# Optimization experiments

Hardware: AMD Instinct MI355X
Metric: run time of the kernel (lower is better)

Reference implementation:

```python
import jax, jax.numpy as jnp
import numpy as np

IN_DIM = 128
SLOT_SIZE = 64
NUM_SLOTS = 8
NUM_ITERS = 3
MLP_HDIM = 128
EPSILON = 1e-08


def _layernorm(x, g, b, eps=1e-5):
    m = jnp.mean(x, axis=-1, keepdims=True)
    v = jnp.mean((x - m) ** 2, axis=-1, keepdims=True)
    return (x - m) * jax.lax.rsqrt(v + eps) * g + b


def setup_inputs() -> dict:
    key = jax.random.key(0)
    ks = jax.random.split(key, 16)
    H, D, K, M = SLOT_SIZE, IN_DIM, NUM_SLOTS, MLP_HDIM
    x = jax.random.normal(ks[0], (32, 4096, D), dtype=jnp.float32)
    noise = jax.random.normal(ks[1], (32, K, H), dtype=jnp.float32)
    s = lambda k, shape, fan_in: jax.random.normal(k, shape, jnp.float32) * (1.0 / np.sqrt(fan_in))
    return {
        'x': x,
        'noise': noise,
        'Wq': s(ks[2], (H, H), H),            # project_q (no bias)
        'Wk': s(ks[3], (H, D), D),            # project_k
        'Wv': s(ks[4], (H, D), D),            # project_v
        'ln_in_g': jnp.ones((D,), jnp.float32), 'ln_in_b': jnp.zeros((D,), jnp.float32),
        'ln_sl_g': jnp.ones((H,), jnp.float32), 'ln_sl_b': jnp.zeros((H,), jnp.float32),
        'ln_mlp_g': jnp.ones((H,), jnp.float32), 'ln_mlp_b': jnp.zeros((H,), jnp.float32),
        'gru_w_ih': s(ks[5], (3 * H, H), H),  # PyTorch GRUCell weight_ih (r,z,n)
        'gru_w_hh': s(ks[6], (3 * H, H), H),
        'gru_b_ih': jnp.zeros((3 * H,), jnp.float32),
        'gru_b_hh': jnp.zeros((3 * H,), jnp.float32),
        'mlp_w1': s(ks[7], (M, H), H), 'mlp_b1': jnp.zeros((M,), jnp.float32),
        'mlp_w2': s(ks[8], (H, M), M), 'mlp_b2': jnp.zeros((H,), jnp.float32),
        'slots_mu': jnp.tile(jnp.linspace(-1.0, 1.0, K, dtype=jnp.float32)[None, :, None], (1, 1, H)),
        'slots_logsigma': jnp.full((1, K, H), -1.0, dtype=jnp.float32),
    }


def reference(x, noise, Wq, Wk, Wv, ln_in_g, ln_in_b, ln_sl_g, ln_sl_b,
              ln_mlp_g, ln_mlp_b, gru_w_ih, gru_w_hh, gru_b_ih, gru_b_hh,
              mlp_w1, mlp_b1, mlp_w2, mlp_b2, slots_mu, slots_logsigma):
    B = x.shape[0]
    H, K = SLOT_SIZE, NUM_SLOTS
    xn = _layernorm(x, ln_in_g, ln_in_b)
    k = jnp.einsum('bnd,hd->bnh', xn, Wk)  # [B,N,H]
    v = jnp.einsum('bnd,hd->bnh', xn, Wv)

    scale = jax.nn.softplus(slots_logsigma) + 1e-05
    slots = slots_mu + scale * noise  # rsample, broadcast over batch -> [B,K,H]

    def step(slots):
        slots_prev = slots
        s = _layernorm(slots, ln_sl_g, ln_sl_b)
        q = jnp.einsum('bkh,gh->bkg', s, Wq)  # [B,K,H]
        scores = (H ** -0.5) * jnp.einsum('bnh,bkh->bnk', k, q)
        attn = jax.nn.softmax(scores, axis=-1) + EPSILON  # softmax over slots
        attn = attn / jnp.sum(attn, axis=1, keepdims=True)  # normalize over inputs
        updates = jnp.einsum('bnk,bnh->bkh', attn, v)
        # PyTorch GRUCell: gates ordered (r, z, n)
        u = updates.reshape(-1, H)
        h = slots_prev.reshape(-1, H)
        gx = u @ gru_w_ih.T + gru_b_ih
        gh = h @ gru_w_hh.T + gru_b_hh
        xr, xz, xn_ = jnp.split(gx, 3, axis=-1)
        hr, hz, hn = jnp.split(gh, 3, axis=-1)
        r = jax.nn.sigmoid(xr + hr)
        z = jax.nn.sigmoid(xz + hz)
        n = jnp.tanh(xn_ + r * hn)
        slots = ((1.0 - z) * n + z * h).reshape(B, K, H)
        slots = _layernorm(slots, ln_mlp_g, ln_mlp_b)
        mlp_out = jax.nn.relu(slots @ mlp_w1.T + mlp_b1) @ mlp_w2.T + mlp_b2
        return slots + mlp_out

    for _ in range(NUM_ITERS):
        slots = step(slots)
    return slots
```

## Files before the change

kernel.cpp:

```cpp
#include <hip/hip_runtime.h>

typedef __attribute__((ext_vector_type(8))) short s16x8;
typedef __attribute__((ext_vector_type(4))) float f32x4;

#define DEV static __device__ __forceinline__

DEV float b2f(unsigned short u){
  unsigned int i = ((unsigned int)u) << 16;
  float f; __builtin_memcpy(&f, &i, 4); return f;
}
DEV unsigned short f2b(float f){
  unsigned int i; __builtin_memcpy(&i, &f, 4);
  i = i + 0x7fffu + ((i >> 16) & 1u);
  return (unsigned short)(i >> 16);
}
DEV f32x4 mfma16(s16x8 a, s16x8 b, f32x4 c){
  return __builtin_amdgcn_mfma_f32_16x16x32_bf16(a, b, c, 0, 0, 0);
}
DEV s16x8 ld8f(const float* p){
  const float4* q4 = (const float4*)p;
  float4 a = q4[0], b = q4[1];
  s16x8 r;
  r[0]=(short)f2b(a.x); r[1]=(short)f2b(a.y); r[2]=(short)f2b(a.z); r[3]=(short)f2b(a.w);
  r[4]=(short)f2b(b.x); r[5]=(short)f2b(b.y); r[6]=(short)f2b(b.z); r[7]=(short)f2b(b.w);
  return r;
}

template<int C> DEV float dpp_addstep(float x){
  int y = __builtin_amdgcn_update_dpp(0, __builtin_bit_cast(int, x), C, 0xF, 0xF, true);
  return x + __builtin_bit_cast(float, y);
}
DEV float rsum16(float v){
  v = dpp_addstep<0xB1>(v);
  v = dpp_addstep<0x4E>(v);
  v = dpp_addstep<0x141>(v);
  v = dpp_addstep<0x140>(v);
  return v;
}

__global__ __launch_bounds__(256) void k_wpack(
    const float* __restrict__ Wk, const float* __restrict__ Wv,
    const float* __restrict__ wih, const float* __restrict__ whh,
    const float* __restrict__ w1, const float* __restrict__ w2,
    const float* __restrict__ Wq,
    unsigned short* __restrict__ wkb, unsigned short* __restrict__ wvb,
    unsigned short* __restrict__ wall)
{
  int t = blockIdx.x * 256 + threadIdx.x;
  int off = t * 4;
  const float* src; unsigned short* dst;
  if      (off <  8192){ src = Wk  + off;         dst = wkb  + off; }
  else if (off < 16384){ src = Wv  + off -  8192; dst = wvb  + off - 8192; }
  else if (off < 28672){ src = wih + off - 16384; dst = wall + off - 16384; }
  else if (off < 40960){ src = whh + off - 28672; dst = wall + off - 16384; }
  else if (off < 49152){ src = w1  + off - 40960; dst = wall + off - 16384; }
  else if (off < 57344){ src = w2  + off - 49152; dst = wall + off - 16384; }
  else                 { src = Wq  + off - 57344; dst = wall + off - 16384; }
  float4 v = *(const float4*)src;
  ushort4 o;
  o.x = f2b(v.x); o.y = f2b(v.y); o.z = f2b(v.z); o.w = f2b(v.w);
  *(ushort4*)dst = o;
}

__global__ __launch_bounds__(256, 4) void k_lnkv5(
    const float* __restrict__ x,
    const unsigned short* __restrict__ wkb,
    const unsigned short* __restrict__ wvb,
    const float* __restrict__ lg,
    const float* __restrict__ lb,
    unsigned short* __restrict__ kg,
    unsigned short* __restrict__ vt,
    const float* __restrict__ noise,
    const float* __restrict__ mu,
    const float* __restrict__ lsg,
    const float* __restrict__ gsl,
    const float* __restrict__ bsl,
    const float* __restrict__ Wq,
    float* __restrict__ slots,
    unsigned short* __restrict__ qws)
{
  __shared__ __align__(16) unsigned int xs[128 * 68];
  const int tid = threadIdx.x;
  const int w = tid >> 6, ln = tid & 63;
  const int m16 = ln & 15, q = ln >> 4;

  if (blockIdx.x >= 1024){
    unsigned short* st = (unsigned short*)xs;
    float (*redS)[4] = (float(*)[4])((char*)xs + 2304);
    float (*redQ)[4] = (float(*)[4])((char*)xs + 2560);
    const int bi = blockIdx.x - 1024;
    const int r0 = bi * 16;
    const int cw = w*16 + m16;

    float sl[4], s1[4], s2[4];
    #pragma unroll
    for (int rr = 0; rr < 4; ++rr){
      int row = r0 + q*4 + rr;
      int k = row & 7;
      float v = mu[k*64 + cw] + (log1pf(expf(lsg[k*64 + cw])) + 1e-5f) * noise[row*64 + cw];
      sl[rr] = v;
      slots[row*64 + cw] = v;
      s1[rr] = rsum16(v);
      s2[rr] = rsum16(v*v);
    }
    if (m16 == 0){
      #pragma unroll
      for (int rr = 0; rr < 4; ++rr){ redS[q*4+rr][w] = s1[rr]; redQ[q*4+rr][w] = s2[rr]; }
    }
    __syncthreads();
    {
      const float gs = gsl[cw], bs = bsl[cw];
      #pragma unroll
      for (int rr = 0; rr < 4; ++rr){
        f32x4 aS = *(const f32x4*)redS[q*4+rr];
        f32x4 aQ = *(const f32x4*)redQ[q*4+rr];
        float tS = aS[0]+aS[1]+aS[2]+aS[3];
        float tQ = aQ[0]+aQ[1]+aQ[2]+aQ[3];
        float mean = tS*(1.f/64.f);
        float var  = tQ*(1.f/64.f) - mean*mean;
        float rs = rsqrtf(var + 1e-5f);
        float sq = (sl[rr] - mean)*rs*gs + bs;
        st[(q*4+rr)*72 + cw] = f2b(sq);
      }
    }
    __syncthreads();
    {
      f32x4 acc = {0,0,0,0};
      #pragma unroll
      for (int ks = 0; ks < 2; ++ks){
        s16x8 a = *(const s16x8*)(st + m16*72 + ks*32 + q*8);
        acc = mfma16(a, ld8f(Wq + cw*64 + ks*32 + q*8), acc);
      }
      #pragma unroll
      for (int rr = 0; rr < 4; ++rr){
        int row = r0 + q*4 + rr;
        int bb_ = row >> 3, kk = row & 7;
        qws[(bb_*16 + kk)*64 + cw] = f2b(acc[rr] * 0.125f);
      }
      int b0 = bi * 2;
      ((unsigned int*)(qws + (b0*16 + 8)*64))[tid] = 0u;
      ((unsigned int*)(qws + ((b0+1)*16 + 8)*64))[tid] = 0u;
    }
    return;
  }

  const int b = blockIdx.x >> 5;
  const int nbase = (blockIdx.x & 31) << 7;
  const long rowg0 = (long)b * 4096 + nbase;

  {
    const int c = m16;
    const float4 gA = *(const float4*)(lg + c*4);
    const float4 gB = *(const float4*)(lg + 64 + c*4);
    const float4 bA = *(const float4*)(lb + c*4);
    const float4 bB = *(const float4*)(lb + 64 + c*4);
    const float* base = x + (rowg0 + w*32 + q)*128;

    float4 va[2], vb[2];
    va[0] = *(const float4*)(base + c*4);
    vb[0] = *(const float4*)(base + 64 + c*4);
    #pragma unroll
    for (int p = 0; p < 8; ++p){
      const int cur = p & 1, nxt = cur ^ 1;
      if (p < 7){
        va[nxt] = *(const float4*)(base + (p+1)*512 + c*4);
        vb[nxt] = *(const float4*)(base + (p+1)*512 + 64 + c*4);
      }
      float4 u = va[cur], t = vb[cur];
      float s1 = (u.x + u.y) + (u.z + u.w) + (t.x + t.y) + (t.z + t.w);
      float s2 = (u.x*u.x + u.y*u.y) + (u.z*u.z + u.w*u.w)
               + (t.x*t.x + t.y*t.y) + (t.z*t.z + t.w*t.w);
      s1 = rsum16(s1);
      s2 = rsum16(s2);
      float mean = s1 * (1.f/128.f);
      float var  = s2 * (1.f/128.f) - mean*mean;
      float rs = rsqrtf(var + 1e-5f);
      float y0 = (u.x - mean)*rs*gA.x + bA.x;
      float y1 = (u.y - mean)*rs*gA.y + bA.y;
      float y2 = (u.z - mean)*rs*gA.z + bA.z;
      float y3 = (u.w - mean)*rs*gA.w + bA.w;
      float y4 = (t.x - mean)*rs*gB.x + bB.x;
      float y5 = (t.y - mean)*rs*gB.y + bB.y;
      float y6 = (t.z - mean)*rs*gB.z + bB.z;
      float y7 = (t.w - mean)*rs*gB.w + bB.w;
      uint2 pkA, pkB;
      pkA.x = (unsigned int)f2b(y0) | ((unsigned int)f2b(y1) << 16);
      pkA.y = (unsigned int)f2b(y2) | ((unsigned int)f2b(y3) << 16);
      pkB.x = (unsigned int)f2b(y4) | ((unsigned int)f2b(y5) << 16);
      pkB.y = (unsigned int)f2b(y6) | ((unsigned int)f2b(y7) << 16);
      const int r = w*32 + p*4 + q;
      *(uint2*)&xs[r*68 + c*2] = pkA;
      *(uint2*)&xs[r*68 + 32 + c*2] = pkB;
    }
  }

  s16x8 bw[4][4];
  #pragma unroll
  for (int t = 0; t < 4; ++t)
    #pragma unroll
    for (int kb = 0; kb < 4; ++kb)
      bw[kb][t] = *(const s16x8*)(wkb + (t*16 + m16)*128 + kb*32 + q*8);

  __syncthreads();

  const f32x4 zf = {0.f, 0.f, 0.f, 0.f};

  #pragma unroll
  for (int mi = 0; mi < 2; ++mi){
    int n0 = (w*2 + mi) * 16;
    f32x4 acc[4];
    #pragma unroll
    for (int t = 0; t < 4; ++t) acc[t] = zf;
    #pragma unroll
    for (int kb = 0; kb < 4; ++kb){
      s16x8 af = *(const s16x8*)((const unsigned short*)(xs + (n0 + m16)*68) + kb*32 + q*8);
      #pragma unroll
      for (int t = 0; t < 4; ++t)
        acc[t] = mfma16(af, bw[kb][t], acc[t]);
    }
    #pragma unroll
    for (int t = 0; t < 4; ++t){
      int h = t*16 + m16;
      #pragma unroll
      for (int rr = 0; rr < 4; ++rr){
        long n = rowg0 + n0 + q*4 + rr;
        kg[n*64 + h] = f2b(acc[t][rr]);
      }
    }
  }

  #pragma unroll
  for (int t = 0; t < 4; ++t)
    #pragma unroll
    for (int kb = 0; kb < 4; ++kb)
      bw[kb][t] = *(const s16x8*)(wvb + (t*16 + m16)*128 + kb*32 + q*8);

  #pragma unroll
  for (int mi = 0; mi < 2; ++mi){
    int n0 = (w*2 + mi) * 16;
    f32x4 acc[4];
    #pragma unroll
    for (int t = 0; t < 4; ++t) acc[t] = zf;
    #pragma unroll
    for (int kb = 0; kb < 4; ++kb){
      s16x8 af = *(const s16x8*)((const unsigned short*)(xs + (n0 + m16)*68) + kb*32 + q*8);
      #pragma unroll
      for (int t = 0; t < 4; ++t)
        acc[t] = mfma16(af, bw[kb][t], acc[t]);
    }
    #pragma unroll
    for (int t = 0; t < 4; ++t){
      int h = t*16 + m16;
      unsigned int p0 = (unsigned int)f2b(acc[t][0]) | ((unsigned int)f2b(acc[t][1]) << 16);
      unsigned int p1 = (unsigned int)f2b(acc[t][2]) | ((unsigned int)f2b(acc[t][3]) << 16);
      uint2 pv; pv.x = p0; pv.y = p1;
      long off = ((long)b*64 + h)*4096 + nbase + n0 + q*4;
      *(uint2*)(vt + off) = pv;
    }
  }
}

__global__ __launch_bounds__(256) void k_attn3(
    const unsigned short* __restrict__ kg,
    const unsigned short* __restrict__ vt,
    const unsigned short* __restrict__ qws,
    const unsigned short* __restrict__ wall,
    const float* __restrict__ bih, const float* __restrict__ bhh,
    const float* __restrict__ b1p, const float* __restrict__ b2p,
    const float* __restrict__ gmlp, const float* __restrict__ bmlp,
    const float* __restrict__ gsl, const float* __restrict__ bsl,
    const float* __restrict__ Up_in, const float* __restrict__ Sp_in,
    float* __restrict__ Up_out, float* __restrict__ Sp_out,
    const float* __restrict__ slin, float* __restrict__ slout,
    int it)
{
  __shared__ float sc[256*17];
  __shared__ unsigned short aT[16*264];
  __shared__ unsigned short ut[16*72], ht[16*72], st[16*72], hid[16*136];
  __shared__ unsigned short qloc[16*72];
  __shared__ __align__(16) float redS[16][4];
  __shared__ __align__(16) float redQ[16][4];
  __shared__ __align__(16) float redS2[16][4];
  __shared__ __align__(16) float redQ2[16][4];

  const int tid = threadIdx.x;
  const int w = tid >> 6, ln = tid & 63;
  const int m16 = ln & 15, q = ln >> 4;
  const int b = blockIdx.x >> 4;
  const int tile = blockIdx.x & 15;
  const int nbase = tile << 8;

  s16x8 afp[4];
  #pragma unroll
  for (int mi = 0; mi < 4; ++mi){
    int n0 = (w*4 + mi)*16;
    afp[mi] = *(const s16x8*)(kg + ((long)b*4096 + nbase + n0 + m16)*64 + q*8);
  }
  s16x8 afp2[4];
  #pragma unroll
  for (int mi = 0; mi < 4; ++mi){
    int n0 = (w*4 + mi)*16;
    afp2[mi] = *(const s16x8*)(kg + ((long)b*4096 + nbase + n0 + m16)*64 + 32 + q*8);
  }
  s16x8 vtp[8];
  #pragma unroll
  for (int ks = 0; ks < 8; ++ks)
    vtp[ks] = *(const s16x8*)(vt + ((long)b*64 + w*16 + m16)*4096 + nbase + ks*32 + q*8);

  for (int i = tid; i < 8*264; i += 256) aT[8*264 + i] = 0;
  if (tid < 128){
    int row = 8 + (tid >> 4), c = (tid & 15)*4;
    ushort4 z4 = {0,0,0,0};
    *(ushort4*)&qloc[row*72 + c] = z4;
  }

  if (it == 0){
    if (tid < 128){
      int row = tid >> 4, c = (tid & 15)*4;
      *(ushort4*)&qloc[row*72 + c] = *(const ushort4*)(qws + (b*16 + row)*64 + c);
    }
  } else {
    const int r0 = (b >> 1) * 16;
    const int cw = w*16 + m16;
    const unsigned short* wihb = wall;
    const unsigned short* whhb = wall + 12288;
    const unsigned short* w1b  = wall + 24576;
    const unsigned short* w2b  = wall + 32768;
    const unsigned short* wqb  = wall + 40960;

    #pragma unroll
    for (int p = 0; p < 4; ++p){
      int row = p*4 + w;
      int g = r0 + row;
      int bb = g >> 3, sl = g & 7;
      const float* up  = Up_in + ((bb*16)*8 + sl)*64 + ln;
      const float* spp = Sp_in + (bb*16)*8 + sl;
      float usum = 0.f, ssum = 0.f;
      #pragma unroll
      for (int t = 0; t < 16; ++t){
        usum += up[t*512];
        ssum += spp[t*8];
      }
      ut[row*72 + ln] = f2b(usum / ssum);
      ht[row*72 + ln] = f2b(slin[g*64 + ln]);
    }
    __syncthreads();

    f32x4 axr = {0,0,0,0}, axz = {0,0,0,0}, axn = {0,0,0,0};
    f32x4 ahr = {0,0,0,0}, ahz = {0,0,0,0}, ahn = {0,0,0,0};
    #pragma unroll
    for (int ks = 0; ks < 2; ++ks){
      s16x8 au = *(const s16x8*)(ut + m16*72 + ks*32 + q*8);
      s16x8 ah = *(const s16x8*)(ht + m16*72 + ks*32 + q*8);
      axr = mfma16(au, *(const s16x8*)(wihb + (      cw)*64 + ks*32 + q*8), axr);
      axz = mfma16(au, *(const s16x8*)(wihb + ( 64 + cw)*64 + ks*32 + q*8), axz);
      axn = mfma16(au, *(const s16x8*)(wihb + (128 + cw)*64 + ks*32 + q*8), axn);
      ahr = mfma16(ah, *(const s16x8*)(whhb + (      cw)*64 + ks*32 + q*8), ahr);
      ahz = mfma16(ah, *(const s16x8*)(whhb + ( 64 + cw)*64 + ks*32 + q*8), ahz);
      ahn = mfma16(ah, *(const s16x8*)(whhb + (128 + cw)*64 + ks*32 + q*8), ahn);
    }
    const float bxr = bih[cw], bxz = bih[64+cw], bxn = bih[128+cw];
    const float bhr = bhh[cw], bhz = bhh[64+cw], bhn = bhh[128+cw];
    float sp[4];
    #pragma unroll
    for (int rr = 0; rr < 4; ++rr){
      float xr = axr[rr] + bxr, xz = axz[rr] + bxz, xnv = axn[rr] + bxn;
      float hr = ahr[rr] + bhr, hz = ahz[rr] + bhz, hn = ahn[rr] + bhn;
      float rg = 1.f / (1.f + expf(-(xr + hr)));
      float zg = 1.f / (1.f + expf(-(xz + hz)));
      float ng = tanhf(xnv + rg*hn);
      float hv = b2f(ht[(q*4 + rr)*72 + cw]);
      sp[rr] = (1.f - zg)*ng + zg*hv;
    }

    float s1[4], s2[4];
    #pragma unroll
    for (int rr = 0; rr < 4; ++rr){
      s1[rr] = rsum16(sp[rr]);
      s2[rr] = rsum16(sp[rr]*sp[rr]);
    }
    if (m16 == 0){
      #pragma unroll
      for (int rr = 0; rr < 4; ++rr){ redS[q*4+rr][w] = s1[rr]; redQ[q*4+rr][w] = s2[rr]; }
    }
    __syncthreads();
    float sl_[4];
    {
      const float gm = gmlp[cw], bm = bmlp[cw];
      #pragma unroll
      for (int rr = 0; rr < 4; ++rr){
        f32x4 aS = *(const f32x4*)redS[q*4+rr];
        f32x4 aQ = *(const f32x4*)redQ[q*4+rr];
        float tS = aS[0]+aS[1]+aS[2]+aS[3];
        float tQ = aQ[0]+aQ[1]+aQ[2]+aQ[3];
        float mean = tS*(1.f/64.f);
        float var  = tQ*(1.f/64.f) - mean*mean;
        float rs = rsqrtf(var + 1e-5f);
        sl_[rr] = (sp[rr] - mean)*rs*gm + bm;
        st[(q*4+rr)*72 + cw] = f2b(sl_[rr]);
      }
    }
    __syncthreads();

    #pragma unroll
    for (int t2 = 0; t2 < 2; ++t2){
      int nt = w*2 + t2;
      int col = nt*16 + m16;
      f32x4 acc = {0,0,0,0};
      #pragma unroll
      for (int ks = 0; ks < 2; ++ks){
        s16x8 a = *(const s16x8*)(st + m16*72 + ks*32 + q*8);
        acc = mfma16(a, *(const s16x8*)(w1b + col*64 + ks*32 + q*8), acc);
      }
      float bb = b1p[col];
      #pragma unroll
      for (int rr = 0; rr < 4; ++rr)
        hid[(q*4+rr)*136 + col] = f2b(fmaxf(acc[rr] + bb, 0.f));
    }
    __syncthreads();

    float snew[4];
    {
      f32x4 acc = {0,0,0,0};
      #pragma unroll
      for (int ks = 0; ks < 4; ++ks){
        s16x8 a = *(const s16x8*)(hid + m16*136 + ks*32 + q*8);
        acc = mfma16(a, *(const s16x8*)(w2b + cw*128 + ks*32 + q*8), acc);
      }
      float bb = b2p[cw];
      #pragma unroll
      for (int rr = 0; rr < 4; ++rr){
        snew[rr] = sl_[rr] + acc[rr] + bb;
        if ((blockIdx.x & 31) == 0)
          slout[(r0 + q*4 + rr)*64 + cw] = snew[rr];
      }
    }

    #pragma unroll
    for (int rr = 0; rr < 4; ++rr){
      s1[rr] = rsum16(snew[rr]);
      s2[rr] = rsum16(snew[rr]*snew[rr]);
    }
    if (m16 == 0){
      #pragma unroll
      for (int rr = 0; rr < 4; ++rr){ redS2[q*4+rr][w] = s1[rr]; redQ2[q*4+rr][w] = s2[rr]; }
    }
    __syncthreads();
    {
      const float gs = gsl[cw], bs = bsl[cw];
      #pragma unroll
      for (int rr = 0; rr < 4; ++rr){
        f32x4 aS = *(const f32x4*)redS2[q*4+rr];
        f32x4 aQ = *(const f32x4*)redQ2[q*4+rr];
        float tS = aS[0]+aS[1]+aS[2]+aS[3];
        float tQ = aQ[0]+aQ[1]+aQ[2]+aQ[3];
        float mean = tS*(1.f/64.f);
        float var  = tQ*(1.f/64.f) - mean*mean;
        float rs = rsqrtf(var + 1e-5f);
        float sq = (snew[rr] - mean)*rs*gs + bs;
        st[(q*4+rr)*72 + cw] = f2b(sq);
      }
    }
    __syncthreads();
    {
      f32x4 acc = {0,0,0,0};
      #pragma unroll
      for (int ks = 0; ks < 2; ++ks){
        s16x8 a = *(const s16x8*)(st + m16*72 + ks*32 + q*8);
        acc = mfma16(a, *(const s16x8*)(wqb + cw*64 + ks*32 + q*8), acc);
      }
      #pragma unroll
      for (int rr = 0; rr < 4; ++rr){
        int rloc = q*4 + rr;
        if ((rloc >> 3) == (b & 1))
          qloc[(rloc & 7)*72 + cw] = f2b(acc[rr] * 0.125f);
      }
    }
  }
  __syncthreads();

  s16x8 bq[2];
  #pragma unroll
  for (int ks = 0; ks < 2; ++ks)
    bq[ks] = *(const s16x8*)(qloc + m16*72 + ks*32 + q*8);

  #pragma unroll
  for (int mi = 0; mi < 4; ++mi){
    int n0 = (w*4 + mi)*16;
    f32x4 acc = {0.f, 0.f, 0.f, 0.f};
    acc = mfma16(afp[mi],  bq[0], acc);
    acc = mfma16(afp2[mi], bq[1], acc);
    #pragma unroll
    for (int rr = 0; rr < 4; ++rr)
      sc[(n0 + q*4 + rr)*17 + m16] = acc[rr];
  }
  __syncthreads();

  {
    int r = tid;
    float a8[8];
    float mx = -1e30f;
    #pragma unroll
    for (int j = 0; j < 8; ++j){ a8[j] = sc[r*17 + j]; mx = fmaxf(mx, a8[j]); }
    float ssum = 0.f;
    #pragma unroll
    for (int j = 0; j < 8; ++j){ a8[j] = expf(a8[j] - mx); ssum += a8[j]; }
    float inv = 1.f/ssum;
    #pragma unroll
    for (int j = 0; j < 8; ++j)
      aT[j*264 + r] = f2b(a8[j]*inv + 1e-8f);
  }
  __syncthreads();

  {
    int j = tid >> 5, c = tid & 31;
    float p = 0.f;
    #pragma unroll
    for (int i = 0; i < 8; ++i) p += b2f(aT[j*264 + c + 32*i]);
    p = rsum16(p);
    p += __shfl_xor(p, 16);
    if ((tid & 31) == 0) Sp_out[(b*16 + tile)*8 + j] = p;
  }

  {
    f32x4 acc = {0.f, 0.f, 0.f, 0.f};
    #pragma unroll
    for (int ks = 0; ks < 8; ++ks){
      s16x8 af = *(const s16x8*)(aT + m16*264 + ks*32 + q*8);
      acc = mfma16(af, vtp[ks], acc);
    }
    float* ub = Up_out + ((b*16 + tile)*8)*64 + w*16 + m16;
    #pragma unroll
    for (int rr = 0; rr < 4; ++rr){
      int slot = q*4 + rr;
      if (slot < 8)
        ub[slot*64] = acc[rr];
    }
  }
}

__global__ __launch_bounds__(256) void k_gru2(
    const float* __restrict__ Up, const float* __restrict__ Sp,
    const float* __restrict__ slots,
    const float* __restrict__ wih, const float* __restrict__ whh,
    const float* __restrict__ bih, const float* __restrict__ bhh,
    const float* __restrict__ w1, const float* __restrict__ b1p,
    const float* __restrict__ w2, const float* __restrict__ b2p,
    const float* __restrict__ gmlp, const float* __restrict__ bmlp,
    float* __restrict__ outp)
{
  __shared__ unsigned short ut[16*72], ht[16*72], st[16*72], hid[16*136];
  __shared__ __align__(16) float redS[16][4];
  __shared__ __align__(16) float redQ[16][4];
  const int tid = threadIdx.x;
  const int w = tid >> 6, ln = tid & 63;
  const int m16 = ln & 15, q = ln >> 4;
  const int r0 = blockIdx.x * 16;
  const int cw = w*16 + m16;

  #pragma unroll
  for (int p = 0; p < 4; ++p){
    int row = p*4 + w;
    int g = r0 + row;
    int bb = g >> 3, sl = g & 7;
    const float* up  = Up + ((bb*16)*8 + sl)*64 + ln;
    const float* spp = Sp + (bb*16)*8 + sl;
    float usum = 0.f, ssum = 0.f;
    #pragma unroll
    for (int t = 0; t < 16; ++t){
      usum += up[t*512];
      ssum += spp[t*8];
    }
    ut[row*72 + ln] = f2b(usum / ssum);
    ht[row*72 + ln] = f2b(slots[g*64 + ln]);
  }
  __syncthreads();

  f32x4 axr = {0,0,0,0}, axz = {0,0,0,0}, axn = {0,0,0,0};
  f32x4 ahr = {0,0,0,0}, ahz = {0,0,0,0}, ahn = {0,0,0,0};
  #pragma unroll
  for (int ks = 0; ks < 2; ++ks){
    s16x8 au = *(const s16x8*)(ut + m16*72 + ks*32 + q*8);
    s16x8 ah = *(const s16x8*)(ht + m16*72 + ks*32 + q*8);
    axr = mfma16(au, ld8f(wih + (      cw)*64 + ks*32 + q*8), axr);
    axz = mfma16(au, ld8f(wih + ( 64 + cw)*64 + ks*32 + q*8), axz);
    axn = mfma16(au, ld8f(wih + (128 + cw)*64 + ks*32 + q*8), axn);
    ahr = mfma16(ah, ld8f(whh + (      cw)*64 + ks*32 + q*8), ahr);
    ahz = mfma16(ah, ld8f(whh + ( 64 + cw)*64 + ks*32 + q*8), ahz);
    ahn = mfma16(ah, ld8f(whh + (128 + cw)*64 + ks*32 + q*8), ahn);
  }
  const float bxr = bih[cw], bxz = bih[64+cw], bxn = bih[128+cw];
  const float bhr = bhh[cw], bhz = bhh[64+cw], bhn = bhh[128+cw];
  float sp[4];
  #pragma unroll
  for (int rr = 0; rr < 4; ++rr){
    float xr = axr[rr] + bxr, xz = axz[rr] + bxz, xnv = axn[rr] + bxn;
    float hr = ahr[rr] + bhr, hz = ahz[rr] + bhz, hn = ahn[rr] + bhn;
    float rg = 1.f / (1.f + expf(-(xr + hr)));
    float zg = 1.f / (1.f + expf(-(xz + hz)));
    float ng = tanhf(xnv + rg*hn);
    float hv = b2f(ht[(q*4 + rr)*72 + cw]);
    sp[rr] = (1.f - zg)*ng + zg*hv;
  }

  float s1[4], s2[4];
  #pragma unroll
  for (int rr = 0; rr < 4; ++rr){
    s1[rr] = rsum16(sp[rr]);
    s2[rr] = rsum16(sp[rr]*sp[rr]);
  }
  if (m16 == 0){
    #pragma unroll
    for (int rr = 0; rr < 4; ++rr){ redS[q*4+rr][w] = s1[rr]; redQ[q*4+rr][w] = s2[rr]; }
  }
  __syncthreads();
  float sl_[4];
  {
    const float gm = gmlp[cw], bm = bmlp[cw];
    #pragma unroll
    for (int rr = 0; rr < 4; ++rr){
      f32x4 aS = *(const f32x4*)redS[q*4+rr];
      f32x4 aQ = *(const f32x4*)redQ[q*4+rr];
      float tS = aS[0]+aS[1]+aS[2]+aS[3];
      float tQ = aQ[0]+aQ[1]+aQ[2]+aQ[3];
      float mean = tS*(1.f/64.f);
      float var  = tQ*(1.f/64.f) - mean*mean;
      float rs = rsqrtf(var + 1e-5f);
      sl_[rr] = (sp[rr] - mean)*rs*gm + bm;
      st[(q*4+rr)*72 + cw] = f2b(sl_[rr]);
    }
  }
  __syncthreads();

  #pragma unroll
  for (int t2 = 0; t2 < 2; ++t2){
    int nt = w*2 + t2;
    int col = nt*16 + m16;
    f32x4 acc = {0,0,0,0};
    #pragma unroll
    for (int ks = 0; ks < 2; ++ks){
      s16x8 a = *(const s16x8*)(st + m16*72 + ks*32 + q*8);
      acc = mfma16(a, ld8f(w1 + col*64 + ks*32 + q*8), acc);
    }
    float bb = b1p[col];
    #pragma unroll
    for (int rr = 0; rr < 4; ++rr)
      hid[(q*4+rr)*136 + col] = f2b(fmaxf(acc[rr] + bb, 0.f));
  }
  __syncthreads();

  {
    f32x4 acc = {0,0,0,0};
    #pragma unroll
    for (int ks = 0; ks < 4; ++ks){
      s16x8 a = *(const s16x8*)(hid + m16*136 + ks*32 + q*8);
      acc = mfma16(a, ld8f(w2 + cw*128 + ks*32 + q*8), acc);
    }
    float bb = b2p[cw];
    #pragma unroll
    for (int rr = 0; rr < 4; ++rr){
      int row = r0 + q*4 + rr;
      outp[row*64 + cw] = sl_[rr] + acc[rr] + bb;
    }
  }
}

extern "C" void kernel_launch(void* const* d_in, const int* in_sizes, int n_in,
                              void* d_out, int out_size, void* d_ws, size_t ws_size,
                              hipStream_t stream)
{
  const float* x    = (const float*)d_in[0];
  const float* noise= (const float*)d_in[1];
  const float* Wq   = (const float*)d_in[2];
  const float* Wk   = (const float*)d_in[3];
  const float* Wv   = (const float*)d_in[4];
  const float* ling = (const float*)d_in[5];
  const float* linb = (const float*)d_in[6];
  const float* gsl  = (const float*)d_in[7];
  const float* bsl  = (const float*)d_in[8];
  const float* gmlp = (const float*)d_in[9];
  const float* bmlp = (const float*)d_in[10];
  const float* wih  = (const float*)d_in[11];
  const float* whh  = (const float*)d_in[12];
  const float* bih  = (const float*)d_in[13];
  const float* bhh  = (const float*)d_in[14];
  const float* w1   = (const float*)d_in[15];
  const float* b1p  = (const float*)d_in[16];
  const float* w2   = (const float*)d_in[17];
  const float* b2p  = (const float*)d_in[18];
  const float* mu   = (const float*)d_in[19];
  const float* lsg  = (const float*)d_in[20];

  char* ws = (char*)d_ws;
  unsigned short* kg   = (unsigned short*)(ws);
  unsigned short* vt   = (unsigned short*)(ws + 16777216);
  char* base = ws + 33554432;
  unsigned short* qws  = (unsigned short*)(base);
  float* slotsA        = (float*)(base + 65536);
  float* slotsB        = (float*)(base + 131072);
  float* slotsC        = (float*)(base + 196608);
  float* UA            = (float*)(base + 262144);
  float* UB            = (float*)(base + 1310720);
  float* SA            = (float*)(base + 2359296);
  float* SB            = (float*)(base + 2375680);
  unsigned short* wkb  = (unsigned short*)(base + 2392064);
  unsigned short* wvb  = (unsigned short*)(base + 2408448);
  unsigned short* wall = (unsigned short*)(base + 2424832);
  float* outp          = (float*)d_out;

  hipLaunchKernelGGL(k_wpack, dim3(60), dim3(256), 0, stream,
                     Wk, Wv, wih, whh, w1, w2, Wq, wkb, wvb, wall);
  hipLaunchKernelGGL(k_lnkv5, dim3(1040), dim3(256), 0, stream,
                     x, wkb, wvb, ling, linb, kg, vt,
                     noise, mu, lsg, gsl, bsl, Wq, slotsA, qws);
  hipLaunchKernelGGL(k_attn3, dim3(512), dim3(256), 0, stream,
                     kg, vt, qws, wall, bih, bhh, b1p, b2p, gmlp, bmlp, gsl, bsl,
                     UA, SA, UA, SA, slotsA, slotsA, 0);
  hipLaunchKernelGGL(k_attn3, dim3(512), dim3(256), 0, stream,
                     kg, vt, qws, wall, bih, bhh, b1p, b2p, gmlp, bmlp, gsl, bsl,
                     UA, SA, UB, SB, slotsA, slotsB, 1);
  hipLaunchKernelGGL(k_attn3, dim3(512), dim3(256), 0, stream,
                     kg, vt, qws, wall, bih, bhh, b1p, b2p, gmlp, bmlp, gsl, bsl,
                     UB, SB, UA, SA, slotsB, slotsC, 2);
  hipLaunchKernelGGL(k_gru2, dim3(16), dim3(256), 0, stream, UA, SA, slotsC,
                     wih, whh, bih, bhh, w1, b1p, w2, b2p, gmlp, bmlp, outp);
  (void)in_sizes; (void)n_in; (void)out_size; (void)ws_size;
}
```

Measured before the change: 201.9 us.

## Fuse three attention iterations and final GRU into one persistent kernel with grid barrier

Replaces the three k_attn3 launches and the k_gru2 launch with a single persistent k_iter kernel that loops over the iterations and separates them with a software grid-wide atomic barrier. The final GRU/MLP runs in the first 16 blocks after the last barrier. K and V fragments are no longer held in registers across phases; they are reloaded from global memory inside each iteration. Triple-buffered U/S partials avoid read/write races across iterations. The aim is to cut kernel-launch gaps and tail effects, at the risk of spin-wait cost, possible deadlock if not all 512 blocks are co-resident, and repeated global loads.

```diff
diff --git a/kernel.cpp b/kernel.cpp
--- a/kernel.cpp
+++ b/kernel.cpp
@@ -38,14 +38,36 @@
   return v;
 }
 
+DEV void gridbar(unsigned int* bar, unsigned int nblk){
+  __syncthreads();
+  if (threadIdx.x == 0){
+    __threadfence();
+    unsigned int g = __hip_atomic_load(&bar[1], __ATOMIC_RELAXED, __HIP_MEMORY_SCOPE_AGENT);
+    unsigned int old = __hip_atomic_fetch_add(&bar[0], 1u, __ATOMIC_ACQ_REL, __HIP_MEMORY_SCOPE_AGENT);
+    if (old == nblk - 1u){
+      __hip_atomic_store(&bar[0], 0u, __ATOMIC_RELAXED, __HIP_MEMORY_SCOPE_AGENT);
+      __hip_atomic_store(&bar[1], g + 1u, __ATOMIC_RELEASE, __HIP_MEMORY_SCOPE_AGENT);
+    } else {
+      int tries = 0;
+      while (__hip_atomic_load(&bar[1], __ATOMIC_ACQUIRE, __HIP_MEMORY_SCOPE_AGENT) == g){
+        if (++tries > (1 << 24)) break;
+      }
+    }
+    __threadfence();
+  }
+  __syncthreads();
+}
+
 __global__ __launch_bounds__(256) void k_wpack(
     const float* __restrict__ Wk, const float* __restrict__ Wv,
     const float* __restrict__ wih, const float* __restrict__ whh,
     const float* __restrict__ w1, const float* __restrict__ w2,
     const float* __restrict__ Wq,
     unsigned short* __restrict__ wkb, unsigned short* __restrict__ wvb,
-    unsigned short* __restrict__ wall)
+    unsigned short* __restrict__ wall,
+    unsigned int* __restrict__ bar)
 {
+  if (blockIdx.x == 0 && threadIdx.x == 0){ bar[0] = 0u; bar[1] = 0u; }
   int t = blockIdx.x * 256 + threadIdx.x;
   int off = t * 4;
   const float* src; unsigned short* dst;
@@ -260,7 +282,7 @@
   }
 }
 
-__global__ __launch_bounds__(256) void k_attn3(
+__global__ __launch_bounds__(256, 4) void k_iter(
     const unsigned short* __restrict__ kg,
     const unsigned short* __restrict__ vt,
     const unsigned short* __restrict__ qws,
@@ -269,10 +291,12 @@
     const float* __restrict__ b1p, const float* __restrict__ b2p,
     const float* __restrict__ gmlp, const float* __restrict__ bmlp,
     const float* __restrict__ gsl, const float* __restrict__ bsl,
-    const float* __restrict__ Up_in, const float* __restrict__ Sp_in,
-    float* __restrict__ Up_out, float* __restrict__ Sp_out,
-    const float* __restrict__ slin, float* __restrict__ slout,
-    int it)
+    float* __restrict__ U0, float* __restrict__ U1, float* __restrict__ U2,
+    float* __restrict__ S0, float* __restrict__ S1, float* __restrict__ S2,
+    float* __restrict__ slotsA, float* __restrict__ slotsB,
+    float* __restrict__ slotsC,
+    float* __restrict__ outp,
+    unsigned int* __restrict__ bar)
 {
   __shared__ float sc[256*17];
   __shared__ unsigned short aT[16*264];
@@ -289,23 +313,13 @@
   const int b = blockIdx.x >> 4;
   const int tile = blockIdx.x & 15;
   const int nbase = tile << 8;
-
-  s16x8 afp[4];
-  #pragma unroll
-  for (int mi = 0; mi < 4; ++mi){
-    int n0 = (w*4 + mi)*16;
-    afp[mi] = *(const s16x8*)(kg + ((long)b*4096 + nbase + n0 + m16)*64 + q*8);
-  }
-  s16x8 afp2[4];
-  #pragma unroll
-  for (int mi = 0; mi < 4; ++mi){
-    int n0 = (w*4 + mi)*16;
-    afp2[mi] = *(const s16x8*)(kg + ((long)b*4096 + nbase + n0 + m16)*64 + 32 + q*8);
-  }
-  s16x8 vtp[8];
-  #pragma unroll
-  for (int ks = 0; ks < 8; ++ks)
-    vtp[ks] = *(const s16x8*)(vt + ((long)b*64 + w*16 + m16)*4096 + nbase + ks*32 + q*8);
+  const int cw = w*16 + m16;
+
+  const unsigned short* wihb = wall;
+  const unsigned short* whhb = wall + 12288;
+  const unsigned short* w1b  = wall + 24576;
+  const unsigned short* w2b  = wall + 32768;
+  const unsigned short* wqb  = wall + 40960;
 
   for (int i = tid; i < 8*264; i += 256) aT[8*264 + i] = 0;
   if (tid < 128){
@@ -314,27 +328,250 @@
     *(ushort4*)&qloc[row*72 + c] = z4;
   }
 
-  if (it == 0){
-    if (tid < 128){
-      int row = tid >> 4, c = (tid & 15)*4;
-      *(ushort4*)&qloc[row*72 + c] = *(const ushort4*)(qws + (b*16 + row)*64 + c);
-    }
-  } else {
-    const int r0 = (b >> 1) * 16;
-    const int cw = w*16 + m16;
-    const unsigned short* wihb = wall;
-    const unsigned short* whhb = wall + 12288;
-    const unsigned short* w1b  = wall + 24576;
-    const unsigned short* w2b  = wall + 32768;
-    const unsigned short* wqb  = wall + 40960;
+  for (int it = 0; it < 3; ++it){
+    const float* Up_in  = (it == 1) ? U0 : U1;
+    const float* Sp_in  = (it == 1) ? S0 : S1;
+    float*       Up_out = (it == 0) ? U0 : ((it == 1) ? U1 : U2);
+    float*       Sp_out = (it == 0) ? S0 : ((it == 1) ? S1 : S2);
+    const float* slin   = (it == 1) ? slotsA : slotsB;
+    float*       slout  = (it == 1) ? slotsB : slotsC;
+
+    if (it == 0){
+      if (tid < 128){
+        int row = tid >> 4, c = (tid & 15)*4;
+        *(ushort4*)&qloc[row*72 + c] = *(const ushort4*)(qws + (b*16 + row)*64 + c);
+      }
+    } else {
+      const int r0 = (b >> 1) * 16;
+
+      #pragma unroll
+      for (int p = 0; p < 4; ++p){
+        int row = p*4 + w;
+        int g = r0 + row;
+        int bb = g >> 3, sl = g & 7;
+        const float* up  = Up_in + ((bb*16)*8 + sl)*64 + ln;
+        const float* spp = Sp_in + (bb*16)*8 + sl;
+        float usum = 0.f, ssum = 0.f;
+        #pragma unroll
+        for (int t = 0; t < 16; ++t){
+          usum += up[t*512];
+          ssum += spp[t*8];
+        }
+        ut[row*72 + ln] = f2b(usum / ssum);
+        ht[row*72 + ln] = f2b(slin[g*64 + ln]);
+      }
+      __syncthreads();
+
+      f32x4 axr = {0,0,0,0}, axz = {0,0,0,0}, axn = {0,0,0,0};
+      f32x4 ahr = {0,0,0,0}, ahz = {0,0,0,0}, ahn = {0,0,0,0};
+      #pragma unroll
+      for (int ks = 0; ks < 2; ++ks){
+        s16x8 au = *(const s16x8*)(ut + m16*72 + ks*32 + q*8);
+        s16x8 ah = *(const s16x8*)(ht + m16*72 + ks*32 + q*8);
+        axr = mfma16(au, *(const s16x8*)(wihb + (      cw)*64 + ks*32 + q*8), axr);
+        axz = mfma16(au, *(const s16x8*)(wihb + ( 64 + cw)*64 + ks*32 + q*8), axz);
+        axn = mfma16(au, *(const s16x8*)(wihb + (128 + cw)*64 + ks*32 + q*8), axn);
+        ahr = mfma16(ah, *(const s16x8*)(whhb + (      cw)*64 + ks*32 + q*8), ahr);
+        ahz = mfma16(ah, *(const s16x8*)(whhb + ( 64 + cw)*64 + ks*32 + q*8), ahz);
+        ahn = mfma16(ah, *(const s16x8*)(whhb + (128 + cw)*64 + ks*32 + q*8), ahn);
+      }
+      const float bxr = bih[cw], bxz = bih[64+cw], bxn = bih[128+cw];
+      const float bhr = bhh[cw], bhz = bhh[64+cw], bhn = bhh[128+cw];
+      float sp[4];
+      #pragma unroll
+      for (int rr = 0; rr < 4; ++rr){
+        float xr = axr[rr] + bxr, xz = axz[rr] + bxz, xnv = axn[rr] + bxn;
+        float hr = ahr[rr] + bhr, hz = ahz[rr] + bhz, hn = ahn[rr] + bhn;
+        float rg = 1.f / (1.f + expf(-(xr + hr)));
+        float zg = 1.f / (1.f + expf(-(xz + hz)));
+        float ng = tanhf(xnv + rg*hn);
+        float hv = b2f(ht[(q*4 + rr)*72 + cw]);
+        sp[rr] = (1.f - zg)*ng + zg*hv;
+      }
+
+      float s1[4], s2[4];
+      #pragma unroll
+      for (int rr = 0; rr < 4; ++rr){
+        s1[rr] = rsum16(sp[rr]);
+        s2[rr] = rsum16(sp[rr]*sp[rr]);
+      }
+      if (m16 == 0){
+        #pragma unroll
+        for (int rr = 0; rr < 4; ++rr){ redS[q*4+rr][w] = s1[rr]; redQ[q*4+rr][w] = s2[rr]; }
+      }
+      __syncthreads();
+      float sl_[4];
+      {
+        const float gm = gmlp[cw], bm = bmlp[cw];
+        #pragma unroll
+        for (int rr = 0; rr < 4; ++rr){
+          f32x4 aS = *(const f32x4*)redS[q*4+rr];
+          f32x4 aQ = *(const f32x4*)redQ[q*4+rr];
+          float tS = aS[0]+aS[1]+aS[2]+aS[3];
+          float tQ = aQ[0]+aQ[1]+aQ[2]+aQ[3];
+          float mean = tS*(1.f/64.f);
+          float var  = tQ*(1.f/64.f) - mean*mean;
+          float rs = rsqrtf(var + 1e-5f);
+          sl_[rr] = (sp[rr] - mean)*rs*gm + bm;
+          st[(q*4+rr)*72 + cw] = f2b(sl_[rr]);
+        }
+      }
+      __syncthreads();
+
+      #pragma unroll
+      for (int t2 = 0; t2 < 2; ++t2){
+        int nt = w*2 + t2;
+        int col = nt*16 + m16;
+        f32x4 acc = {0,0,0,0};
+        #pragma unroll
+        for (int ks = 0; ks < 2; ++ks){
+          s16x8 a = *(const s16x8*)(st + m16*72 + ks*32 + q*8);
+          acc = mfma16(a, *(const s16x8*)(w1b + col*64 + ks*32 + q*8), acc);
+        }
+        float bb = b1p[col];
+        #pragma unroll
+        for (int rr = 0; rr < 4; ++rr)
+          hid[(q*4+rr)*136 + col] = f2b(fmaxf(acc[rr] + bb, 0.f));
+      }
+      __syncthreads();
+
+      float snew[4];
+      {
+        f32x4 acc = {0,0,0,0};
+        #pragma unroll
+        for (int ks = 0; ks < 4; ++ks){
+          s16x8 a = *(const s16x8*)(hid + m16*136 + ks*32 + q*8);
+          acc = mfma16(a, *(const s16x8*)(w2b + cw*128 + ks*32 + q*8), acc);
+        }
+        float bb = b2p[cw];
+        #pragma unroll
+        for (int rr = 0; rr < 4; ++rr){
+          snew[rr] = sl_[rr] + acc[rr] + bb;
+          if ((blockIdx.x & 31) == 0)
+            slout[(r0 + q*4 + rr)*64 + cw] = snew[rr];
+        }
+      }
+
+      #pragma unroll
+      for (int rr = 0; rr < 4; ++rr){
+        s1[rr] = rsum16(snew[rr]);
+        s2[rr] = rsum16(snew[rr]*snew[rr]);
+      }
+      if (m16 == 0){
+        #pragma unroll
+        for (int rr = 0; rr < 4; ++rr){ redS2[q*4+rr][w] = s1[rr]; redQ2[q*4+rr][w] = s2[rr]; }
+      }
+      __syncthreads();
+      {
+        const float gs = gsl[cw], bs = bsl[cw];
+        #pragma unroll
+        for (int rr = 0; rr < 4; ++rr){
+          f32x4 aS = *(const f32x4*)redS2[q*4+rr];
+          f32x4 aQ = *(const f32x4*)redQ2[q*4+rr];
+          float tS = aS[0]+aS[1]+aS[2]+aS[3];
+          float tQ = aQ[0]+aQ[1]+aQ[2]+aQ[3];
+          float mean = tS*(1.f/64.f);
+          float var  = tQ*(1.f/64.f) - mean*mean;
+          float rs = rsqrtf(var + 1e-5f);
+          float sq = (snew[rr] - mean)*rs*gs + bs;
+          st[(q*4+rr)*72 + cw] = f2b(sq);
+        }
+      }
+      __syncthreads();
+      {
+        f32x4 acc = {0,0,0,0};
+        #pragma unroll
+        for (int ks = 0; ks < 2; ++ks){
+          s16x8 a = *(const s16x8*)(st + m16*72 + ks*32 + q*8);
+          acc = mfma16(a, *(const s16x8*)(wqb + cw*64 + ks*32 + q*8), acc);
+        }
+        #pragma unroll
+        for (int rr = 0; rr < 4; ++rr){
+          int rloc = q*4 + rr;
+          if ((rloc >> 3) == (b & 1))
+            qloc[(rloc & 7)*72 + cw] = f2b(acc[rr] * 0.125f);
+        }
+      }
+    }
+    __syncthreads();
+
+    s16x8 bq[2];
+    #pragma unroll
+    for (int ks = 0; ks < 2; ++ks)
+      bq[ks] = *(const s16x8*)(qloc + m16*72 + ks*32 + q*8);
+
+    #pragma unroll
+    for (int mi = 0; mi < 4; ++mi){
+      int n0 = (w*4 + mi)*16;
+      f32x4 acc = {0.f, 0.f, 0.f, 0.f};
+      #pragma unroll
+      for (int ks = 0; ks < 2; ++ks){
+        s16x8 af = *(const s16x8*)(kg + ((long)b*4096 + nbase + n0 + m16)*64 + ks*32 + q*8);
+        acc = mfma16(af, bq[ks], acc);
+      }
+      #pragma unroll
+      for (int rr = 0; rr < 4; ++rr)
+        sc[(n0 + q*4 + rr)*17 + m16] = acc[rr];
+    }
+    __syncthreads();
+
+    {
+      int r = tid;
+      float a8[8];
+      float mx = -1e30f;
+      #pragma unroll
+      for (int j = 0; j < 8; ++j){ a8[j] = sc[r*17 + j]; mx = fmaxf(mx, a8[j]); }
+      float ssum = 0.f;
+      #pragma unroll
+      for (int j = 0; j < 8; ++j){ a8[j] = expf(a8[j] - mx); ssum += a8[j]; }
+      float inv = 1.f/ssum;
+      #pragma unroll
+      for (int j = 0; j < 8; ++j)
+        aT[j*264 + r] = f2b(a8[j]*inv + 1e-8f);
+    }
+    __syncthreads();
+
+    {
+      int j = tid >> 5, c = tid & 31;
+      float p = 0.f;
+      #pragma unroll
+      for (int i = 0; i < 8; ++i) p += b2f(aT[j*264 + c + 32*i]);
+      p = rsum16(p);
+      p += __shfl_xor(p, 16);
+      if ((tid & 31) == 0) Sp_out[(b*16 + tile)*8 + j] = p;
+    }
+
+    {
+      f32x4 acc = {0.f, 0.f, 0.f, 0.f};
+      #pragma unroll
+      for (int ks = 0; ks < 8; ++ks){
+        s16x8 af = *(const s16x8*)(aT + m16*264 + ks*32 + q*8);
+        s16x8 bf = *(const s16x8*)(vt + ((long)b*64 + w*16 + m16)*4096 + nbase + ks*32 + q*8);
+        acc = mfma16(af, bf, acc);
+      }
+      float* ub = Up_out + ((b*16 + tile)*8)*64 + w*16 + m16;
+      #pragma unroll
+      for (int rr = 0; rr < 4; ++rr){
+        int slot = q*4 + rr;
+        if (slot < 8)
+          ub[slot*64] = acc[rr];
+      }
+    }
+
+    gridbar(bar, 512u);
+  }
+
+  if (blockIdx.x >= 16) return;
+  {
+    const int r0 = blockIdx.x * 16;
 
     #pragma unroll
     for (int p = 0; p < 4; ++p){
       int row = p*4 + w;
       int g = r0 + row;
       int bb = g >> 3, sl = g & 7;
-      const float* up  = Up_in + ((bb*16)*8 + sl)*64 + ln;
-      const float* spp = Sp_in + (bb*16)*8 + sl;
+      const float* up  = U2 + ((bb*16)*8 + sl)*64 + ln;
+      const float* spp = S2 + (bb*16)*8 + sl;
       float usum = 0.f, ssum = 0.f;
       #pragma unroll
       for (int t = 0; t < 16; ++t){
@@ -342,7 +579,7 @@
         ssum += spp[t*8];
       }
       ut[row*72 + ln] = f2b(usum / ssum);
-      ht[row*72 + ln] = f2b(slin[g*64 + ln]);
+      ht[row*72 + ln] = f2b(slotsC[g*64 + ln]);
     }
     __syncthreads();
 
@@ -419,7 +656,6 @@
     }
     __syncthreads();
 
-    float snew[4];
     {
       f32x4 acc = {0,0,0,0};
       #pragma unroll
@@ -430,237 +666,9 @@
       float bb = b2p[cw];
       #pragma unroll
       for (int rr = 0; rr < 4; ++rr){
-        snew[rr] = sl_[rr] + acc[rr] + bb;
-        if ((blockIdx.x & 31) == 0)
-          slout[(r0 + q*4 + rr)*64 + cw] = snew[rr];
-      }
-    }
-
-    #pragma unroll
-    for (int rr = 0; rr < 4; ++rr){
-      s1[rr] = rsum16(snew[rr]);
-      s2[rr] = rsum16(snew[rr]*snew[rr]);
-    }
-    if (m16 == 0){
-      #pragma unroll
-      for (int rr = 0; rr < 4; ++rr){ redS2[q*4+rr][w] = s1[rr]; redQ2[q*4+rr][w] = s2[rr]; }
-    }
-    __syncthreads();
-    {
-      const float gs = gsl[cw], bs = bsl[cw];
-      #pragma unroll
-      for (int rr = 0; rr < 4; ++rr){
-        f32x4 aS = *(const f32x4*)redS2[q*4+rr];
-        f32x4 aQ = *(const f32x4*)redQ2[q*4+rr];
-        float tS = aS[0]+aS[1]+aS[2]+aS[3];
-        float tQ = aQ[0]+aQ[1]+aQ[2]+aQ[3];
-        float mean = tS*(1.f/64.f);
-        float var  = tQ*(1.f/64.f) - mean*mean;
-        float rs = rsqrtf(var + 1e-5f);
-        float sq = (snew[rr] - mean)*rs*gs + bs;
-        st[(q*4+rr)*72 + cw] = f2b(sq);
-      }
-    }
-    __syncthreads();
-    {
-      f32x4 acc = {0,0,0,0};
-      #pragma unroll
-      for (int ks = 0; ks < 2; ++ks){
-        s16x8 a = *(const s16x8*)(st + m16*72 + ks*32 + q*8);
-        acc = mfma16(a, *(const s16x8*)(wqb + cw*64 + ks*32 + q*8), acc);
-      }
-      #pragma unroll
-      for (int rr = 0; rr < 4; ++rr){
-        int rloc = q*4 + rr;
-        if ((rloc >> 3) == (b & 1))
-          qloc[(rloc & 7)*72 + cw] = f2b(acc[rr] * 0.125f);
-      }
-    }
-  }
-  __syncthreads();
-
-  s16x8 bq[2];
-  #pragma unroll
-  for (int ks = 0; ks < 2; ++ks)
-    bq[ks] = *(const s16x8*)(qloc + m16*72 + ks*32 + q*8);
-
-  #pragma unroll
-  for (int mi = 0; mi < 4; ++mi){
-    int n0 = (w*4 + mi)*16;
-    f32x4 acc = {0.f, 0.f, 0.f, 0.f};
-    acc = mfma16(afp[mi],  bq[0], acc);
-    acc = mfma16(afp2[mi], bq[1], acc);
-    #pragma unroll
-    for (int rr = 0; rr < 4; ++rr)
-      sc[(n0 + q*4 + rr)*17 + m16] = acc[rr];
-  }
-  __syncthreads();
-
-  {
-    int r = tid;
-    float a8[8];
-    float mx = -1e30f;
-    #pragma unroll
-    for (int j = 0; j < 8; ++j){ a8[j] = sc[r*17 + j]; mx = fmaxf(mx, a8[j]); }
-    float ssum = 0.f;
-    #pragma unroll
-    for (int j = 0; j < 8; ++j){ a8[j] = expf(a8[j] - mx); ssum += a8[j]; }
-    float inv = 1.f/ssum;
-    #pragma unroll
-    for (int j = 0; j < 8; ++j)
-      aT[j*264 + r] = f2b(a8[j]*inv + 1e-8f);
-  }
-  __syncthreads();
-
-  {
-    int j = tid >> 5, c = tid & 31;
-    float p = 0.f;
-    #pragma unroll
-    for (int i = 0; i < 8; ++i) p += b2f(aT[j*264 + c + 32*i]);
-    p = rsum16(p);
-    p += __shfl_xor(p, 16);
-    if ((tid & 31) == 0) Sp_out[(b*16 + tile)*8 + j] = p;
-  }
-
-  {
-    f32x4 acc = {0.f, 0.f, 0.f, 0.f};
-    #pragma unroll
-    for (int ks = 0; ks < 8; ++ks){
-      s16x8 af = *(const s16x8*)(aT + m16*264 + ks*32 + q*8);
-      acc = mfma16(af, vtp[ks], acc);
-    }
-    float* ub = Up_out + ((b*16 + tile)*8)*64 + w*16 + m16;
-    #pragma unroll
-    for (int rr = 0; rr < 4; ++rr){
-      int slot = q*4 + rr;
-      if (slot < 8)
-        ub[slot*64] = acc[rr];
-    }
-  }
-}
-
-__global__ __launch_bounds__(256) void k_gru2(
-    const float* __restrict__ Up, const float* __restrict__ Sp,
-    const float* __restrict__ slots,
-    const float* __restrict__ wih, const float* __restrict__ whh,
-    const float* __restrict__ bih, const float* __restrict__ bhh,
-    const float* __restrict__ w1, const float* __restrict__ b1p,
-    const float* __restrict__ w2, const float* __restrict__ b2p,
-    const float* __restrict__ gmlp, const float* __restrict__ bmlp,
-    float* __restrict__ outp)
-{
-  __shared__ unsigned short ut[16*72], ht[16*72], st[16*72], hid[16*136];
-  __shared__ __align__(16) float redS[16][4];
-  __shared__ __align__(16) float redQ[16][4];
-  const int tid = threadIdx.x;
-  const int w = tid >> 6, ln = tid & 63;
-  const int m16 = ln & 15, q = ln >> 4;
-  const int r0 = blockIdx.x * 16;
-  const int cw = w*16 + m16;
-
-  #pragma unroll
-  for (int p = 0; p < 4; ++p){
-    int row = p*4 + w;
-    int g = r0 + row;
-    int bb = g >> 3, sl = g & 7;
-    const float* up  = Up + ((bb*16)*8 + sl)*64 + ln;
-    const float* spp = Sp + (bb*16)*8 + sl;
-    float usum = 0.f, ssum = 0.f;
-    #pragma unroll
-    for (int t = 0; t < 16; ++t){
-      usum += up[t*512];
-      ssum += spp[t*8];
-    }
-    ut[row*72 + ln] = f2b(usum / ssum);
-    ht[row*72 + ln] = f2b(slots[g*64 + ln]);
-  }
-  __syncthreads();
-
-  f32x4 axr = {0,0,0,0}, axz = {0,0,0,0}, axn = {0,0,0,0};
-  f32x4 ahr = {0,0,0,0}, ahz = {0,0,0,0}, ahn = {0,0,0,0};
-  #pragma unroll
-  for (int ks = 0; ks < 2; ++ks){
-    s16x8 au = *(const s16x8*)(ut + m16*72 + ks*32 + q*8);
-    s16x8 ah = *(const s16x8*)(ht + m16*72 + ks*32 + q*8);
-    axr = mfma16(au, ld8f(wih + (      cw)*64 + ks*32 + q*8), axr);
-    axz = mfma16(au, ld8f(wih + ( 64 + cw)*64 + ks*32 + q*8), axz);
-    axn = mfma16(au, ld8f(wih + (128 + cw)*64 + ks*32 + q*8), axn);
-    ahr = mfma16(ah, ld8f(whh + (      cw)*64 + ks*32 + q*8), ahr);
-    ahz = mfma16(ah, ld8f(whh + ( 64 + cw)*64 + ks*32 + q*8), ahz);
-    ahn = mfma16(ah, ld8f(whh + (128 + cw)*64 + ks*32 + q*8), ahn);
-  }
-  const float bxr = bih[cw], bxz = bih[64+cw], bxn = bih[128+cw];
-  const float bhr = bhh[cw], bhz = bhh[64+cw], bhn = bhh[128+cw];
-  float sp[4];
-  #pragma unroll
-  for (int rr = 0; rr < 4; ++rr){
-    float xr = axr[rr] + bxr, xz = axz[rr] + bxz, xnv = axn[rr] + bxn;
-    float hr = ahr[rr] + bhr, hz = ahz[rr] + bhz, hn = ahn[rr] + bhn;
-    float rg = 1.f / (1.f + expf(-(xr + hr)));
-    float zg = 1.f / (1.f + expf(-(xz + hz)));
-    float ng = tanhf(xnv + rg*hn);
-    float hv = b2f(ht[(q*4 + rr)*72 + cw]);
-    sp[rr] = (1.f - zg)*ng + zg*hv;
-  }
-
-  float s1[4], s2[4];
-  #pragma unroll
-  for (int rr = 0; rr < 4; ++rr){
-    s1[rr] = rsum16(sp[rr]);
-    s2[rr] = rsum16(sp[rr]*sp[rr]);
-  }
-  if (m16 == 0){
-    #pragma unroll
-    for (int rr = 0; rr < 4; ++rr){ redS[q*4+rr][w] = s1[rr]; redQ[q*4+rr][w] = s2[rr]; }
-  }
-  __syncthreads();
-  float sl_[4];
-  {
-    const float gm = gmlp[cw], bm = bmlp[cw];
-    #pragma unroll
-    for (int rr = 0; rr < 4; ++rr){
-      f32x4 aS = *(const f32x4*)redS[q*4+rr];
-      f32x4 aQ = *(const f32x4*)redQ[q*4+rr];
-      float tS = aS[0]+aS[1]+aS[2]+aS[3];
-      float tQ = aQ[0]+aQ[1]+aQ[2]+aQ[3];
-      float mean = tS*(1.f/64.f);
-      float var  = tQ*(1.f/64.f) - mean*mean;
-      float rs = rsqrtf(var + 1e-5f);
-      sl_[rr] = (sp[rr] - mean)*rs*gm + bm;
-      st[(q*4+rr)*72 + cw] = f2b(sl_[rr]);
-    }
-  }
-  __syncthreads();
-
-  #pragma unroll
-  for (int t2 = 0; t2 < 2; ++t2){
-    int nt = w*2 + t2;
-    int col = nt*16 + m16;
-    f32x4 acc = {0,0,0,0};
-    #pragma unroll
-    for (int ks = 0; ks < 2; ++ks){
-      s16x8 a = *(const s16x8*)(st + m16*72 + ks*32 + q*8);
-      acc = mfma16(a, ld8f(w1 + col*64 + ks*32 + q*8), acc);
-    }
-    float bb = b1p[col];
-    #pragma unroll
-    for (int rr = 0; rr < 4; ++rr)
-      hid[(q*4+rr)*136 + col] = f2b(fmaxf(acc[rr] + bb, 0.f));
-  }
-  __syncthreads();
-
-  {
-    f32x4 acc = {0,0,0,0};
-    #pragma unroll
-    for (int ks = 0; ks < 4; ++ks){
-      s16x8 a = *(const s16x8*)(hid + m16*136 + ks*32 + q*8);
-      acc = mfma16(a, ld8f(w2 + cw*128 + ks*32 + q*8), acc);
-    }
-    float bb = b2p[cw];
-    #pragma unroll
-    for (int rr = 0; rr < 4; ++rr){
-      int row = r0 + q*4 + rr;
-      outp[row*64 + cw] = sl_[rr] + acc[rr] + bb;
+        int row = r0 + q*4 + rr;
+        outp[row*64 + cw] = sl_[rr] + acc[rr] + bb;
+      }
     }
   }
 }
@@ -699,30 +707,27 @@
   float* slotsA        = (float*)(base + 65536);
   float* slotsB        = (float*)(base + 131072);
   float* slotsC        = (float*)(base + 196608);
-  float* UA            = (float*)(base + 262144);
-  float* UB            = (float*)(base + 1310720);
-  float* SA            = (float*)(base + 2359296);
-  float* SB            = (float*)(base + 2375680);
-  unsigned short* wkb  = (unsigned short*)(base + 2392064);
-  unsigned short* wvb  = (unsigned short*)(base + 2408448);
-  unsigned short* wall = (unsigned short*)(base + 2424832);
+  float* U0            = (float*)(base + 262144);
+  float* U1            = (float*)(base + 1310720);
+  float* U2            = (float*)(base + 2359296);
+  float* S0            = (float*)(base + 3407872);
+  float* S1            = (float*)(base + 3424256);
+  float* S2            = (float*)(base + 3440640);
+  unsigned short* wkb  = (unsigned short*)(base + 3457024);
+  unsigned short* wvb  = (unsigned short*)(base + 3473408);
+  unsigned short* wall = (unsigned short*)(base + 3489792);
+  unsigned int* bar    = (unsigned int*)(base + 3579904);
   float* outp          = (float*)d_out;
 
   hipLaunchKernelGGL(k_wpack, dim3(60), dim3(256), 0, stream,
-                     Wk, Wv, wih, whh, w1, w2, Wq, wkb, wvb, wall);
+                     Wk, Wv, wih, whh, w1, w2, Wq, wkb, wvb, wall, bar);
   hipLaunchKernelGGL(k_lnkv5, dim3(1040), dim3(256), 0, stream,
                      x, wkb, wvb, ling, linb, kg, vt,
                      noise, mu, lsg, gsl, bsl, Wq, slotsA, qws);
-  hipLaunchKernelGGL(k_attn3, dim3(512), dim3(256), 0, stream,
-                     kg, vt, qws, wall, bih, bhh, b1p, b2p, gmlp, bmlp, gsl, bsl,
-                     UA, SA, UA, SA, slotsA, slotsA, 0);
-  hipLaunchKernelGGL(k_attn3, dim3(512), dim3(256), 0, stream,
-                     kg, vt, qws, wall, bih, bhh, b1p, b2p, gmlp, bmlp, gsl, bsl,
-                     UA, SA, UB, SB, slotsA, slotsB, 1);
-  hipLaunchKernelGGL(k_attn3, dim3(512), dim3(256), 0, stream,
-                     kg, vt, qws, wall, bih, bhh, b1p, b2p, gmlp, bmlp, gsl, bsl,
-                     UB, SB, UA, SA, slotsB, slotsC, 2);
-  hipLaunchKernelGGL(k_gru2, dim3(16), dim3(256), 0, stream, UA, SA, slotsC,
-                     wih, whh, bih, bhh, w1, b1p, w2, b2p, gmlp, bmlp, outp);
+  hipLaunchKernelGGL(k_iter, dim3(512), dim3(256), 0, stream,
+                     kg, vt, qws, wall, bih, bhh, b1p, b2p,
+                     gmlp, bmlp, gsl, bsl,
+                     U0, U1, U2, S0, S1, S2,
+                     slotsA, slotsB, slotsC, outp, bar);
   (void)in_sizes; (void)n_in; (void)out_size; (void)ws_size;
 }
```

Result: slower. 485.4 us (+140.4%).
